# Performance work log

Measured on AMD Instinct MI355X. Metric: run time of the kernel, lower is better.

Reference implementation:

```python
import jax, jax.numpy as jnp
import numpy as np

N = 50000
E = 600000
FEAT = 32
ACT = 8
H = 128
HEADS = 4
C = H // HEADS
L = 3
NEG_SLOPE = 0.2
LN_EPS = 1e-5


def setup_inputs() -> dict:
    key = jax.random.key(0)
    ks = jax.random.split(key, 32)
    s = 0.05
    inp = {
        'x': jax.random.normal(ks[0], (N, FEAT), jnp.float32),
        'action': jax.random.normal(ks[1], (N, ACT), jnp.float32),
        'edge_index': jax.random.randint(ks[2], (2, E), 0, N, jnp.int32),
        # node encoder: Linear(feat+act -> H) + LayerNorm
        'W0': jax.random.normal(ks[3], (FEAT + ACT, H), jnp.float32) * s,
        'b0': jnp.zeros((H,), jnp.float32),
        'ln0_g': jnp.ones((H,), jnp.float32),
        'ln0_b': jnp.zeros((H,), jnp.float32),
        # GAT layers (stacked over L): lin W [L,H,heads*C], att vectors, bias, LayerNorm
        'Wg': jax.random.normal(ks[4], (L, H, HEADS * C), jnp.float32) * s,
        'att_src': jax.random.normal(ks[5], (L, HEADS, C), jnp.float32) * s,
        'att_dst': jax.random.normal(ks[6], (L, HEADS, C), jnp.float32) * s,
        'bg': jnp.zeros((L, HEADS * C), jnp.float32),
        'lng_g': jnp.ones((L, H), jnp.float32),
        'lng_b': jnp.zeros((L, H), jnp.float32),
        # dynamics head
        'Wd1': jax.random.normal(ks[7], (H, H), jnp.float32) * s,
        'bd1': jnp.zeros((H,), jnp.float32),
        'Wd2': jax.random.normal(ks[8], (H, FEAT), jnp.float32) * s,
        'bd2': jnp.zeros((FEAT,), jnp.float32),
        # reward head
        'Wr1': jax.random.normal(ks[9], (H, H // 2), jnp.float32) * s,
        'br1': jnp.zeros((H // 2,), jnp.float32),
        'Wr2': jax.random.normal(ks[10], (H // 2, 1), jnp.float32) * s,
        'br2': jnp.zeros((1,), jnp.float32),
        # constraint head
        'Wc1': jax.random.normal(ks[11], (H, H // 2), jnp.float32) * s,
        'bc1': jnp.zeros((H // 2,), jnp.float32),
        'Wc2': jax.random.normal(ks[12], (H // 2, 1), jnp.float32) * s,
        'bc2': jnp.zeros((1,), jnp.float32),
    }
    return inp


def _layernorm(x, g, b):
    mu = jnp.mean(x, axis=-1, keepdims=True)
    var = jnp.mean(jnp.square(x - mu), axis=-1, keepdims=True)
    return (x - mu) * jax.lax.rsqrt(var + LN_EPS) * g + b


def _gat_layer(h, src, dst, W, a_src, a_dst, bias):
    # PyG GATConv: xp = lin(h) per head; alpha = leaky_relu(a_src.x_j + a_dst.x_i)
    xp = (h @ W).reshape(N, HEADS, C)                    # [N, heads, C]
    s_src = jnp.sum(xp * a_src, axis=-1)                 # [N, heads]
    s_dst = jnp.sum(xp * a_dst, axis=-1)                 # [N, heads]
    alpha = jax.nn.leaky_relu(s_src[src] + s_dst[dst], NEG_SLOPE)  # [E', heads]
    # segment softmax over edges grouped by destination node
    amax = jax.ops.segment_max(alpha, dst, num_segments=N)
    ex = jnp.exp(alpha - amax[dst])
    den = jax.ops.segment_sum(ex, dst, num_segments=N)
    attn = ex / den[dst]                                 # [E', heads]
    msg = xp[src] * attn[..., None]                      # [E', heads, C]
    out = jax.ops.segment_sum(msg.reshape(-1, HEADS * C), dst, num_segments=N)
    return out + bias                                    # [N, H]


def reference(x, action, edge_index, W0, b0, ln0_g, ln0_b, Wg, att_src, att_dst,
              bg, lng_g, lng_b, Wd1, bd1, Wd2, bd2, Wr1, br1, Wr2, br2,
              Wc1, bc1, Wc2, bc2):
    # add self loops (PyG GATConv default)
    loops = jnp.arange(N, dtype=edge_index.dtype)
    src = jnp.concatenate([edge_index[0], loops])
    dst = jnp.concatenate([edge_index[1], loops])

    h = jax.nn.relu(_layernorm(jnp.concatenate([x, action], axis=-1) @ W0 + b0, ln0_g, ln0_b))
    for l in range(L):
        h_new = _gat_layer(h, src, dst, Wg[l], att_src[l], att_dst[l], bg[l])
        h_new = jax.nn.relu(_layernorm(h_new, lng_g[l], lng_b[l]))
        h = h + h_new

    delta_x = jax.nn.relu(h @ Wd1 + bd1) @ Wd2 + bd2
    next_x = x + delta_x
    graph_emb = jnp.mean(h, axis=0, keepdims=True)       # global_mean_pool, single graph
    reward = (jax.nn.relu(graph_emb @ Wr1 + br1) @ Wr2 + br2).squeeze(-1)
    constraint_prob = jax.nn.sigmoid(jax.nn.relu(graph_emb @ Wc1 + bc1) @ Wc2 + bc2).squeeze(-1)
    return delta_x, next_x, reward, constraint_prob
```

## Files before the change

### kernel.cpp

```cpp
#include <hip/hip_runtime.h>

typedef unsigned short u16;
typedef __attribute__((ext_vector_type(8))) short bf16x8;
typedef __attribute__((ext_vector_type(4))) float f32x4;

#define NN 50000
#define EE 600000
#define EP 650000
#define LNEPS 1e-5f
#define NB 196

__device__ __forceinline__ float bf2f(u16 u) {
    union { unsigned int i; float f; } v; v.i = ((unsigned int)u) << 16; return v.f;
}
__device__ __forceinline__ u16 f2bf(float f) {
    union { float f; unsigned int i; } v; v.f = f;
    unsigned int x = v.i;
    unsigned int r = x + 0x7fffu + ((x >> 16) & 1u);
    return (u16)(r >> 16);
}
__device__ __forceinline__ float ldf(const void* p, long i, int bf) {
    return bf ? bf2f(((const u16*)p)[i]) : ((const float*)p)[i];
}
__device__ __forceinline__ void stf(void* p, long i, int bf, float v) {
    if (bf) ((u16*)p)[i] = f2bf(v); else ((float*)p)[i] = v;
}

#define WTOT 93858
#define BSWN 65536
struct P22 { const void* p[22]; };

__global__ __launch_bounds__(256) void init7(P22 w, float* __restrict__ wf,
                                             u16* __restrict__ bsw,
                                             int* __restrict__ deg,
                                             float* __restrict__ gacc,
                                             int* __restrict__ flag) {
    const unsigned w0 = *(const unsigned*)w.p[2];
    const int bf = (w0 == 0x3F803F80u) ? 1 : 0;
    int i = blockIdx.x * 256 + threadIdx.x;
    if (i < WTOT) {
        const int offs[23] = {0,5120,5248,5376,5504,54656,55040,55424,55808,56192,56576,
                              72960,73088,77184,77216,85408,85472,85536,85537,93729,93793,
                              93857,93858};
        int seg = 0;
        while (offs[seg + 1] <= i) ++seg;
        wf[i] = ldf(w.p[seg], i - offs[seg], bf);
        return;
    }
    i -= WTOT;
    if (i < BSWN) {
        int mat = i >> 14, rem = i & 16383;
        int ct = rem >> 11, r2 = rem & 2047;
        int kb = r2 >> 9, r3 = r2 & 511;
        int lane = r3 >> 3, j = r3 & 7;
        int k = kb * 32 + (lane >> 4) * 8 + j;
        int n = ct * 16 + (lane & 15);
        float v = (mat < 3) ? ldf(w.p[4], (long)mat * 16384 + (long)k * 128 + n, bf)
                            : ldf(w.p[10], (long)k * 128 + n, bf);
        bsw[i] = f2bf(v);
        return;
    }
    i -= BSWN;
    if (i < NN) { deg[i] = 0; return; }
    i -= NN;
    if (i < 128) { gacc[i] = 0.f; return; }
    if (i == 128) *flag = bf;
}

__global__ __launch_bounds__(256) void enc6(
    const void* __restrict__ x, const void* __restrict__ act,
    const float* __restrict__ wf, u16* __restrict__ hb,
    const int* __restrict__ flg) {
    const float* W0f = wf;
    const float* b0f = wf + 5120;
    const float* gf  = wf + 5248;
    const float* bbf = wf + 5376;
    __shared__ float As[32][41];
    const int bf = *flg;
    int t = threadIdx.x;
    int r0 = blockIdx.x * 32;
    #pragma unroll
    for (int i = 0; i < 5; ++i) {
        int idx = t + i * 256;
        int r = idx / 40, k = idx - r * 40;
        int rr = r0 + r; if (rr >= NN) rr = NN - 1;
        As[r][k] = (k < 32) ? ldf(x, (long)rr * 32 + k, bf)
                            : ldf(act, (long)rr * 8 + (k - 32), bf);
    }
    __syncthreads();
    int colq = t & 31, mq = t >> 5;
    int col0 = colq * 4;
    float4 b0v = *(const float4*)(b0f + col0);
    float acc[4][4];
    #pragma unroll
    for (int j = 0; j < 4; ++j) {
        acc[j][0] = b0v.x; acc[j][1] = b0v.y; acc[j][2] = b0v.z; acc[j][3] = b0v.w;
    }
    #pragma unroll 2
    for (int k = 0; k < 40; ++k) {
        float4 b4 = *(const float4*)(W0f + k * 128 + col0);
        float a0 = As[mq * 4 + 0][k];
        float a1 = As[mq * 4 + 1][k];
        float a2 = As[mq * 4 + 2][k];
        float a3 = As[mq * 4 + 3][k];
        acc[0][0] += a0 * b4.x; acc[0][1] += a0 * b4.y; acc[0][2] += a0 * b4.z; acc[0][3] += a0 * b4.w;
        acc[1][0] += a1 * b4.x; acc[1][1] += a1 * b4.y; acc[1][2] += a1 * b4.z; acc[1][3] += a1 * b4.w;
        acc[2][0] += a2 * b4.x; acc[2][1] += a2 * b4.y; acc[2][2] += a2 * b4.z; acc[2][3] += a2 * b4.w;
        acc[3][0] += a3 * b4.x; acc[3][1] += a3 * b4.y; acc[3][2] += a3 * b4.z; acc[3][3] += a3 * b4.w;
    }
    float4 gv = *(const float4*)(gf + col0);
    float4 bv = *(const float4*)(bbf + col0);
    #pragma unroll
    for (int j = 0; j < 4; ++j) {
        int row = r0 + mq * 4 + j;
        float pa = acc[j][0] + acc[j][1] + acc[j][2] + acc[j][3];
        #pragma unroll
        for (int o = 1; o <= 16; o <<= 1) pa += __shfl_xor(pa, o, 32);
        float mu = pa * (1.f / 128.f);
        float d0 = acc[j][0] - mu, d1 = acc[j][1] - mu;
        float d2 = acc[j][2] - mu, d3 = acc[j][3] - mu;
        float q = d0 * d0 + d1 * d1 + d2 * d2 + d3 * d3;
        #pragma unroll
        for (int o = 1; o <= 16; o <<= 1) q += __shfl_xor(q, o, 32);
        float rs = rsqrtf(q * (1.f / 128.f) + LNEPS);
        if (row < NN) {
            ushort4 hbv;
            hbv.x = f2bf(fmaxf(d0 * rs * gv.x + bv.x, 0.f));
            hbv.y = f2bf(fmaxf(d1 * rs * gv.y + bv.y, 0.f));
            hbv.z = f2bf(fmaxf(d2 * rs * gv.z + bv.z, 0.f));
            hbv.w = f2bf(fmaxf(d3 * rs * gv.w + bv.w, 0.f));
            *(ushort4*)(hb + (long)row * 128 + col0) = hbv;
        }
    }
}

__global__ __launch_bounds__(256) void lin7(
    const u16* __restrict__ hb, const u16* __restrict__ bswm,
    const float* __restrict__ bias, u16* __restrict__ out, int dorelu,
    int doscore, const float* __restrict__ wf, int layer,
    float* __restrict__ s_src, float* __restrict__ s_dst,
    int douth, const void* __restrict__ x, void* __restrict__ dout,
    const int* __restrict__ flg) {
    __shared__ u16 As[32 * 136];
    __shared__ u16 ts[32 * 136];
    int t = threadIdx.x;
    int r0 = blockIdx.x * 32;
    #pragma unroll
    for (int i = 0; i < 2; ++i) {
        int idx = (t + i * 256) * 8;
        int r = idx >> 7, k = idx & 127;
        int rr = r0 + r; if (rr >= NN) rr = NN - 1;
        int4 v = *(const int4*)(hb + (long)rr * 128 + k);
        *(int4*)(As + r * 136 + k) = v;
    }
    __syncthreads();
    int w = t >> 6, lane = t & 63;
    int rt = w & 1, ctbase = (w >> 1) * 4;
    int quad = lane >> 4, l15 = lane & 15;
    int rowl = rt * 16 + l15;
    bf16x8 afr[4];
    #pragma unroll
    for (int kb = 0; kb < 4; ++kb)
        afr[kb] = *(const bf16x8*)(As + rowl * 136 + kb * 32 + quad * 8);
    const float* asrf = wf + 54656 + layer * 128;
    const float* adsf = wf + 55040 + layer * 128;
    int headbase = (w >> 1) * 2;
    #pragma unroll
    for (int cp = 0; cp < 2; ++cp) {
        int ct0 = ctbase + cp * 2, ct1 = ct0 + 1;
        f32x4 acc0 = {0.f, 0.f, 0.f, 0.f};
        f32x4 acc1 = {0.f, 0.f, 0.f, 0.f};
        #pragma unroll
        for (int kb = 0; kb < 4; ++kb) {
            bf16x8 b0 = *(const bf16x8*)(bswm + ct0 * 2048 + kb * 512 + lane * 8);
            acc0 = __builtin_amdgcn_mfma_f32_16x16x32_bf16(afr[kb], b0, acc0, 0, 0, 0);
        }
        #pragma unroll
        for (int kb = 0; kb < 4; ++kb) {
            bf16x8 b1 = *(const bf16x8*)(bswm + ct1 * 2048 + kb * 512 + lane * 8);
            acc1 = __builtin_amdgcn_mfma_f32_16x16x32_bf16(afr[kb], b1, acc1, 0, 0, 0);
        }
        int col0 = ct0 * 16 + l15, col1 = ct1 * 16 + l15;
        float bia0 = dorelu ? bias[col0] : 0.f;
        float bia1 = dorelu ? bias[col1] : 0.f;
        #pragma unroll
        for (int reg = 0; reg < 4; ++reg) {
            int lrow = rt * 16 + quad * 4 + reg;
            int grow = r0 + lrow;
            float z0 = acc0[reg] + bia0, z1 = acc1[reg] + bia1;
            if (dorelu) { z0 = fmaxf(z0, 0.f); z1 = fmaxf(z1, 0.f); }
            if (douth) {
                ts[lrow * 136 + col0] = f2bf(z0);
                ts[lrow * 136 + col1] = f2bf(z1);
            } else if (grow < NN) {
                out[(long)grow * 128 + col0] = f2bf(z0);
                out[(long)grow * 128 + col1] = f2bf(z1);
            }
        }
        if (doscore) {
            float av0 = asrf[col0], av1 = asrf[col1];
            float dv0 = adsf[col0], dv1 = adsf[col1];
            #pragma unroll
            for (int reg = 0; reg < 4; ++reg) {
                float pa = acc0[reg] * av0 + acc1[reg] * av1;
                float pb = acc0[reg] * dv0 + acc1[reg] * dv1;
                #pragma unroll
                for (int o = 1; o <= 8; o <<= 1) {
                    pa += __shfl_xor(pa, o, 64);
                    pb += __shfl_xor(pb, o, 64);
                }
                if (l15 == 0) {
                    int grow = r0 + rt * 16 + quad * 4 + reg;
                    if (grow < NN) {
                        s_src[grow * 4 + headbase + cp] = pa;
                        s_dst[grow * 4 + headbase + cp] = pb;
                    }
                }
            }
        }
    }
    if (douth) {
        __syncthreads();
        const float* Wd2f = wf + 73088;
        const float* bd2f = wf + 77184;
        const int bf = *flg;
        int c = t & 31, mq = t >> 5;
        float acc[4];
        #pragma unroll
        for (int j = 0; j < 4; ++j) acc[j] = bd2f[c];
        #pragma unroll 4
        for (int k = 0; k < 128; ++k) {
            float wv = Wd2f[k * 32 + c];
            acc[0] += bf2f(ts[(mq * 4 + 0) * 136 + k]) * wv;
            acc[1] += bf2f(ts[(mq * 4 + 1) * 136 + k]) * wv;
            acc[2] += bf2f(ts[(mq * 4 + 2) * 136 + k]) * wv;
            acc[3] += bf2f(ts[(mq * 4 + 3) * 136 + k]) * wv;
        }
        #pragma unroll
        for (int j = 0; j < 4; ++j) {
            int node = r0 + mq * 4 + j;
            if (node >= NN) continue;
            stf(dout, (long)node * 32 + c, bf, acc[j]);
            stf(dout, (long)NN * 32 + (long)node * 32 + c, bf,
                ldf(x, (long)node * 32 + c, bf) + acc[j]);
        }
    }
}

__global__ void count3(const int* __restrict__ ei, int* __restrict__ deg) {
    int e = blockIdx.x * 256 + threadIdx.x; if (e >= EP) return;
    int d = (e < EE) ? ei[EE + e] : (e - EE);
    atomicAdd(&deg[d], 1);
}

__global__ __launch_bounds__(256) void scanA(const int* __restrict__ deg,
                                             int* __restrict__ bsum) {
    __shared__ int red[256];
    int t = threadIdx.x; int i = blockIdx.x * 256 + t;
    red[t] = (i < NN) ? deg[i] : 0; __syncthreads();
    for (int s = 128; s >= 1; s >>= 1) { if (t < s) red[t] += red[t + s]; __syncthreads(); }
    if (t == 0) bsum[blockIdx.x] = red[0];
}

__global__ __launch_bounds__(256) void scanB(const int* __restrict__ bsum,
                                             int* __restrict__ boff,
                                             int* __restrict__ offs) {
    __shared__ int sh[256];
    int t = threadIdx.x;
    sh[t] = (t < NB) ? bsum[t] : 0; __syncthreads();
    for (int o = 1; o < 256; o <<= 1) {
        int v = (t >= o) ? sh[t - o] : 0;
        __syncthreads();
        sh[t] += v;
        __syncthreads();
    }
    if (t < NB) boff[t] = (t == 0) ? 0 : sh[t - 1];
    if (t == 0) offs[NN] = EP;
}

__global__ __launch_bounds__(256) void scanC(const int* __restrict__ deg,
                                             const int* __restrict__ boff,
                                             int* __restrict__ offs,
                                             int* __restrict__ cursor) {
    __shared__ int sh[256];
    int t = threadIdx.x; int i = blockIdx.x * 256 + t;
    int v = (i < NN) ? deg[i] : 0;
    sh[t] = v; __syncthreads();
    for (int o = 1; o < 256; o <<= 1) {
        int u = (t >= o) ? sh[t - o] : 0;
        __syncthreads();
        sh[t] += u;
        __syncthreads();
    }
    if (i < NN) {
        int excl = boff[blockIdx.x] + sh[t] - v;
        offs[i] = excl; cursor[i] = excl;
    }
}

__global__ void scatter5(const int* __restrict__ ei, int* __restrict__ cursor,
                         int* __restrict__ csrc) {
    int e = blockIdx.x * 256 + threadIdx.x; if (e >= EP) return;
    int s, d;
    if (e < EE) { s = ei[e]; d = ei[EE + e]; } else { s = e - EE; d = s; }
    int p = atomicAdd(&cursor[d], 1);
    csrc[p] = s;
}

__global__ __launch_bounds__(256) void agg9(
    const u16* __restrict__ xp, const float* __restrict__ s_src,
    const float* __restrict__ s_dst,
    const int* __restrict__ csrc, const int* __restrict__ offs,
    const float* __restrict__ wf, int layer, u16* __restrict__ hb) {
    const float* bgf = wf + 55424 + layer * 128;
    const float* gf  = wf + 55808 + layer * 128;
    const float* bbf = wf + 56192 + layer * 128;
    int t = threadIdx.x;
    int lane = t & 63;
    int n = blockIdx.x * 4 + (t >> 6);
    int q = (lane >> 4) & 3;
    int l16 = lane & 15;
    int c0 = l16 * 8;
    int hd = l16 >> 2;
    int eh = l16 & 3;
    long idx0 = (long)n * 128 + c0;
    int4 hold = *(const int4*)(hb + idx0);
    float sdn_eh = s_dst[n * 4 + eh];
    float sdn_hd = s_dst[n * 4 + hd];
    int beg = offs[n], end = offs[n + 1];
    float a[8] = {};
    float den = 0.f;
    int j = beg;
    for (; j + 8 <= end; j += 8) {
        int s0 = csrc[j + q];
        int s1 = csrc[j + 4 + q];
        int sp0 = csrc[j + hd];
        int sp1 = csrc[j + 4 + hd];
        float aw0 = s_src[sp0 * 4 + eh] + sdn_eh;
        float aw1 = s_src[sp1 * 4 + eh] + sdn_eh;
        aw0 = (aw0 > 0.f) ? aw0 : 0.2f * aw0;
        aw1 = (aw1 > 0.f) ? aw1 : 0.2f * aw1;
        float w0p = __expf(aw0);
        float w1p = __expf(aw1);
        int4 v0 = *(const int4*)(xp + (long)s0 * 128 + c0);
        int4 v1 = *(const int4*)(xp + (long)s1 * 128 + c0);
        float w0 = __shfl(w0p, q * 4 + hd, 64);
        float w1 = __shfl(w1p, q * 4 + hd, 64);
        union { int4 i; u16 u[8]; } u0, u1;
        u0.i = v0; u1.i = v1;
        #pragma unroll
        for (int k = 0; k < 8; ++k)
            a[k] += w0 * bf2f(u0.u[k]) + w1 * bf2f(u1.u[k]);
        den += w0 + w1;
    }
    for (int jj = j + q; jj < end; jj += 4) {
        int s = csrc[jj];
        float aw = s_src[s * 4 + hd] + sdn_hd;
        aw = (aw > 0.f) ? aw : 0.2f * aw;
        float w = __expf(aw);
        int4 v = *(const int4*)(xp + (long)s * 128 + c0);
        union { int4 i; u16 u[8]; } uv; uv.i = v;
        #pragma unroll
        for (int k = 0; k < 8; ++k) a[k] += w * bf2f(uv.u[k]);
        den += w;
    }
    #pragma unroll
    for (int k = 0; k < 8; ++k) {
        a[k] += __shfl_xor(a[k], 16, 64);
        a[k] += __shfl_xor(a[k], 32, 64);
    }
    den += __shfl_xor(den, 16, 64);
    den += __shfl_xor(den, 32, 64);
    float inv = 1.f / den;
    float4 bg0 = *(const float4*)(bgf + c0);
    float4 bg1 = *(const float4*)(bgf + c0 + 4);
    float v[8];
    v[0] = a[0] * inv + bg0.x; v[1] = a[1] * inv + bg0.y;
    v[2] = a[2] * inv + bg0.z; v[3] = a[3] * inv + bg0.w;
    v[4] = a[4] * inv + bg1.x; v[5] = a[5] * inv + bg1.y;
    v[6] = a[6] * inv + bg1.z; v[7] = a[7] * inv + bg1.w;
    float pa = v[0] + v[1] + v[2] + v[3] + v[4] + v[5] + v[6] + v[7];
    #pragma unroll
    for (int o = 1; o <= 8; o <<= 1) pa += __shfl_xor(pa, o, 16);
    float mu = pa * (1.f / 128.f);
    float d[8];
    float qv = 0.f;
    #pragma unroll
    for (int k = 0; k < 8; ++k) { d[k] = v[k] - mu; qv += d[k] * d[k]; }
    #pragma unroll
    for (int o = 1; o <= 8; o <<= 1) qv += __shfl_xor(qv, o, 16);
    float rs = rsqrtf(qv * (1.f / 128.f) + LNEPS);
    float4 g0 = *(const float4*)(gf + c0);
    float4 g1 = *(const float4*)(gf + c0 + 4);
    float4 b0 = *(const float4*)(bbf + c0);
    float4 b1 = *(const float4*)(bbf + c0 + 4);
    float gg[8]  = {g0.x, g0.y, g0.z, g0.w, g1.x, g1.y, g1.z, g1.w};
    float bbv[8] = {b0.x, b0.y, b0.z, b0.w, b1.x, b1.y, b1.z, b1.w};
    if (lane < 16) {
        union { int4 i; u16 u[8]; } hv, ho;
        ho.i = hold;
        #pragma unroll
        for (int k = 0; k < 8; ++k) {
            float y = fmaxf(d[k] * rs * gg[k] + bbv[k], 0.f);
            hv.u[k] = f2bf(bf2f(ho.u[k]) + y);
        }
        *(int4*)(hb + idx0) = hv.i;
    }
}

__global__ __launch_bounds__(128) void pool4(const u16* __restrict__ hb, float* __restrict__ gacc) {
    int c = threadIdx.x;
    int n0 = blockIdx.x * 128;
    float s = 0.f;
    for (int i = 0; i < 128; ++i) {
        int n = n0 + i;
        if (n < NN) s += bf2f(hb[(long)n * 128 + c]);
    }
    atomicAdd(&gacc[c], s);
}

__global__ __launch_bounds__(128) void head4(
    const float* __restrict__ gacc, const float* __restrict__ wf,
    void* __restrict__ out, const int* __restrict__ flg) {
    const float* Wr1f = wf + 77216;
    const float* br1f = wf + 85408;
    const float* Wr2f = wf + 85472;
    const float* br2f = wf + 85536;
    const float* Wc1f = wf + 85537;
    const float* bc1f = wf + 93729;
    const float* Wc2f = wf + 93793;
    const float* bc2f = wf + 93857;
    __shared__ float ge[128];
    __shared__ float hr[128];
    const int bf = *flg;
    int t = threadIdx.x;
    ge[t] = gacc[t] * (1.f / (float)NN);
    __syncthreads();
    {
        int j = t & 63;
        const float* W = (t < 64) ? Wr1f : Wc1f;
        const float* bb = (t < 64) ? br1f : bc1f;
        float a = bb[j];
        for (int k = 0; k < 128; ++k) a += ge[k] * W[k * 64 + j];
        hr[t] = fmaxf(a, 0.f);
    }
    __syncthreads();
    if (t == 0) {
        float r = br2f[0];
        for (int j = 0; j < 64; ++j) r += hr[j] * Wr2f[j];
        stf(out, (long)2 * NN * 32, bf, r);
    } else if (t == 1) {
        float z = bc2f[0];
        for (int j = 0; j < 64; ++j) z += hr[64 + j] * Wc2f[j];
        float p = 1.f / (1.f + __expf(-z));
        stf(out, (long)2 * NN * 32 + 1, bf, p);
    }
}

extern "C" void kernel_launch(void* const* d_in, const int* in_sizes, int n_in,
                              void* d_out, int out_size, void* d_ws, size_t ws_size,
                              hipStream_t stream) {
    const void* x   = d_in[0];
    const void* act = d_in[1];
    const int*  ei  = (const int*)d_in[2];

    char* ws = (char*)d_ws;
    size_t off = 0;
    auto alloc = [&](size_t bytes) -> char* {
        char* p = ws + off;
        off = (off + bytes + 255) & ~(size_t)255;
        return p;
    };
    u16*       hb     = (u16*)      alloc((size_t)NN * 128 * 2);
    u16*       xp     = (u16*)      alloc((size_t)NN * 128 * 2);
    float*     s_src  = (float*)    alloc((size_t)NN * 4 * 4);
    float*     s_dst  = (float*)    alloc((size_t)NN * 4 * 4);
    int*       deg    = (int*)      alloc((size_t)NN * 4);
    int*       cursor = (int*)      alloc((size_t)NN * 4);
    int*       offs   = (int*)      alloc((size_t)(NN + 1) * 4);
    int*       csrc   = (int*)      alloc((size_t)EP * 4);
    float*     wf     = (float*)    alloc((size_t)WTOT * 4);
    u16*       bsw    = (u16*)      alloc((size_t)BSWN * 2);
    float*     gacc   = (float*)    alloc(128 * 4);
    int*       flag   = (int*)      alloc(4);
    int*       bsum   = (int*)      alloc((size_t)NB * 4);
    int*       boff   = (int*)      alloc((size_t)NB * 4);

    P22 wp;
    for (int i = 0; i < 22; ++i) wp.p[i] = d_in[3 + i];
    const int initN = WTOT + BSWN + NN + 129;
    init7<<<(initN + 255) / 256, 256, 0, stream>>>(wp, wf, bsw, deg, gacc, flag);

    const int gemm_blocks = (NN + 31) / 32;
    enc6<<<gemm_blocks, 256, 0, stream>>>(x, act, wf, hb, flag);

    count3<<<(EP + 255) / 256, 256, 0, stream>>>(ei, deg);
    scanA<<<NB, 256, 0, stream>>>(deg, bsum);
    scanB<<<1, 256, 0, stream>>>(bsum, boff, offs);
    scanC<<<NB, 256, 0, stream>>>(deg, boff, offs, cursor);
    scatter5<<<(EP + 255) / 256, 256, 0, stream>>>(ei, cursor, csrc);

    for (int l = 0; l < 3; ++l) {
        lin7<<<gemm_blocks, 256, 0, stream>>>(hb, bsw + (size_t)l * 16384,
                                              (const float*)nullptr, xp, 0,
                                              1, wf, l, s_src, s_dst,
                                              0, x, d_out, flag);
        agg9<<<NN / 4, 256, 0, stream>>>(xp, s_src, s_dst, csrc, offs,
                                         wf, l, hb);
    }

    lin7<<<gemm_blocks, 256, 0, stream>>>(hb, bsw + (size_t)3 * 16384,
                                          wf + 72960, xp, 1,
                                          0, wf, 0, s_src, s_dst,
                                          1, x, d_out, flag);

    pool4<<<(NN + 127) / 128, 128, 0, stream>>>(hb, gacc);
    head4<<<1, 128, 0, stream>>>(gacc, wf, d_out, flag);

    (void)in_sizes; (void)n_in; (void)out_size; (void)ws_size;
}
```

Baseline: 412.9 us.

## Fuse degree count into encoder, merge scan kernels, batch edge loads in aggregation

```diff
diff --git a/kernel.cpp b/kernel.cpp
--- a/kernel.cpp
+++ b/kernel.cpp
@@ -9,6 +9,8 @@
 #define EP 650000
 #define LNEPS 1e-5f
 #define NB 196
+#define ENCB 1563
+#define CNTB 2540
 
 __device__ __forceinline__ float bf2f(u16 u) {
     union { unsigned int i; float f; } v; v.i = ((unsigned int)u) << 16; return v.f;
@@ -67,10 +69,19 @@
     if (i == 128) *flag = bf;
 }
 
-__global__ __launch_bounds__(256) void enc6(
+__global__ __launch_bounds__(256) void enc7(
     const void* __restrict__ x, const void* __restrict__ act,
     const float* __restrict__ wf, u16* __restrict__ hb,
-    const int* __restrict__ flg) {
+    const int* __restrict__ flg, const int* __restrict__ ei,
+    int* __restrict__ deg) {
+    if (blockIdx.x >= ENCB) {
+        int e = (blockIdx.x - ENCB) * 256 + threadIdx.x;
+        if (e < EP) {
+            int d = (e < EE) ? ei[EE + e] : (e - EE);
+            atomicAdd(&deg[d], 1);
+        }
+        return;
+    }
     const float* W0f = wf;
     const float* b0f = wf + 5120;
     const float* gf  = wf + 5248;
@@ -247,12 +258,6 @@
     }
 }
 
-__global__ void count3(const int* __restrict__ ei, int* __restrict__ deg) {
-    int e = blockIdx.x * 256 + threadIdx.x; if (e >= EP) return;
-    int d = (e < EE) ? ei[EE + e] : (e - EE);
-    atomicAdd(&deg[d], 1);
-}
-
 __global__ __launch_bounds__(256) void scanA(const int* __restrict__ deg,
                                              int* __restrict__ bsum) {
     __shared__ int red[256];
@@ -262,40 +267,37 @@
     if (t == 0) bsum[blockIdx.x] = red[0];
 }
 
-__global__ __launch_bounds__(256) void scanB(const int* __restrict__ bsum,
-                                             int* __restrict__ boff,
-                                             int* __restrict__ offs) {
+__global__ __launch_bounds__(256) void scanC2(const int* __restrict__ deg,
+                                              const int* __restrict__ bsum,
+                                              int* __restrict__ offs,
+                                              int* __restrict__ cursor) {
     __shared__ int sh[256];
     int t = threadIdx.x;
-    sh[t] = (t < NB) ? bsum[t] : 0; __syncthreads();
-    for (int o = 1; o < 256; o <<= 1) {
-        int v = (t >= o) ? sh[t - o] : 0;
-        __syncthreads();
-        sh[t] += v;
-        __syncthreads();
-    }
-    if (t < NB) boff[t] = (t == 0) ? 0 : sh[t - 1];
-    if (t == 0) offs[NN] = EP;
-}
-
-__global__ __launch_bounds__(256) void scanC(const int* __restrict__ deg,
-                                             const int* __restrict__ boff,
-                                             int* __restrict__ offs,
-                                             int* __restrict__ cursor) {
-    __shared__ int sh[256];
-    int t = threadIdx.x; int i = blockIdx.x * 256 + t;
-    int v = (i < NN) ? deg[i] : 0;
-    sh[t] = v; __syncthreads();
+    sh[t] = (t < NB) ? bsum[t] : 0;
+    __syncthreads();
     for (int o = 1; o < 256; o <<= 1) {
         int u = (t >= o) ? sh[t - o] : 0;
         __syncthreads();
         sh[t] += u;
         __syncthreads();
     }
+    int pre = (blockIdx.x == 0) ? 0 : sh[blockIdx.x - 1];
+    __syncthreads();
+    int i = blockIdx.x * 256 + t;
+    int v = (i < NN) ? deg[i] : 0;
+    sh[t] = v;
+    __syncthreads();
+    for (int o = 1; o < 256; o <<= 1) {
+        int u = (t >= o) ? sh[t - o] : 0;
+        __syncthreads();
+        sh[t] += u;
+        __syncthreads();
+    }
     if (i < NN) {
-        int excl = boff[blockIdx.x] + sh[t] - v;
+        int excl = pre + sh[t] - v;
         offs[i] = excl; cursor[i] = excl;
     }
+    if (i == 0) offs[NN] = EP;
 }
 
 __global__ void scatter5(const int* __restrict__ ei, int* __restrict__ cursor,
@@ -307,7 +309,7 @@
     csrc[p] = s;
 }
 
-__global__ __launch_bounds__(256) void agg9(
+__global__ __launch_bounds__(256) void agg10(
     const u16* __restrict__ xp, const float* __restrict__ s_src,
     const float* __restrict__ s_dst,
     const int* __restrict__ csrc, const int* __restrict__ offs,
@@ -322,47 +324,41 @@
     int l16 = lane & 15;
     int c0 = l16 * 8;
     int hd = l16 >> 2;
-    int eh = l16 & 3;
     long idx0 = (long)n * 128 + c0;
     int4 hold = *(const int4*)(hb + idx0);
-    float sdn_eh = s_dst[n * 4 + eh];
-    float sdn_hd = s_dst[n * 4 + hd];
+    float sdn = s_dst[n * 4 + (lane & 3)];
     int beg = offs[n], end = offs[n + 1];
     float a[8] = {};
     float den = 0.f;
-    int j = beg;
-    for (; j + 8 <= end; j += 8) {
-        int s0 = csrc[j + q];
-        int s1 = csrc[j + 4 + q];
-        int sp0 = csrc[j + hd];
-        int sp1 = csrc[j + 4 + hd];
-        float aw0 = s_src[sp0 * 4 + eh] + sdn_eh;
-        float aw1 = s_src[sp1 * 4 + eh] + sdn_eh;
-        aw0 = (aw0 > 0.f) ? aw0 : 0.2f * aw0;
-        aw1 = (aw1 > 0.f) ? aw1 : 0.2f * aw1;
-        float w0p = __expf(aw0);
-        float w1p = __expf(aw1);
-        int4 v0 = *(const int4*)(xp + (long)s0 * 128 + c0);
-        int4 v1 = *(const int4*)(xp + (long)s1 * 128 + c0);
-        float w0 = __shfl(w0p, q * 4 + hd, 64);
-        float w1 = __shfl(w1p, q * 4 + hd, 64);
-        union { int4 i; u16 u[8]; } u0, u1;
-        u0.i = v0; u1.i = v1;
-        #pragma unroll
-        for (int k = 0; k < 8; ++k)
-            a[k] += w0 * bf2f(u0.u[k]) + w1 * bf2f(u1.u[k]);
-        den += w0 + w1;
-    }
-    for (int jj = j + q; jj < end; jj += 4) {
-        int s = csrc[jj];
-        float aw = s_src[s * 4 + hd] + sdn_hd;
-        aw = (aw > 0.f) ? aw : 0.2f * aw;
-        float w = __expf(aw);
-        int4 v = *(const int4*)(xp + (long)s * 128 + c0);
-        union { int4 i; u16 u[8]; } uv; uv.i = v;
-        #pragma unroll
-        for (int k = 0; k < 8; ++k) a[k] += w * bf2f(uv.u[k]);
-        den += w;
+    for (int cbeg = beg; cbeg < end; cbeg += 64) {
+        int cdeg = end - cbeg; if (cdeg > 64) cdeg = 64;
+        int eidx = (lane < cdeg) ? csrc[cbeg + lane] : n;
+        for (int base = 0; base < cdeg; base += 16) {
+            int me = base + (lane >> 2);
+            int sm = __shfl(eidx, me & 63, 64);
+            float aw = s_src[sm * 4 + (lane & 3)] + sdn;
+            aw = (aw > 0.f) ? aw : 0.2f * aw;
+            float wv = (me < cdeg) ? __expf(aw) : 0.f;
+            int s00 = __shfl(eidx, base + q, 64);
+            int s01 = __shfl(eidx, base + 4 + q, 64);
+            int s10 = __shfl(eidx, base + 8 + q, 64);
+            int s11 = __shfl(eidx, base + 12 + q, 64);
+            int4 v00 = *(const int4*)(xp + (long)s00 * 128 + c0);
+            int4 v01 = *(const int4*)(xp + (long)s01 * 128 + c0);
+            int4 v10 = *(const int4*)(xp + (long)s10 * 128 + c0);
+            int4 v11 = *(const int4*)(xp + (long)s11 * 128 + c0);
+            float w00 = __shfl(wv, (q << 2) | hd, 64);
+            float w01 = __shfl(wv, ((4 + q) << 2) | hd, 64);
+            float w10 = __shfl(wv, ((8 + q) << 2) | hd, 64);
+            float w11 = __shfl(wv, ((12 + q) << 2) | hd, 64);
+            union { int4 i; u16 u[8]; } u00, u01, u10, u11;
+            u00.i = v00; u01.i = v01; u10.i = v10; u11.i = v11;
+            #pragma unroll
+            for (int k = 0; k < 8; ++k)
+                a[k] += w00 * bf2f(u00.u[k]) + w01 * bf2f(u01.u[k])
+                      + w10 * bf2f(u10.u[k]) + w11 * bf2f(u11.u[k]);
+            den += w00 + w01 + w10 + w11;
+        }
     }
     #pragma unroll
     for (int k = 0; k < 8; ++k) {
@@ -485,34 +481,32 @@
     int*       flag   = (int*)      alloc(4);
     int*       bsum   = (int*)      alloc((size_t)NB * 4);
     int*       boff   = (int*)      alloc((size_t)NB * 4);
+    (void)boff;
 
     P22 wp;
     for (int i = 0; i < 22; ++i) wp.p[i] = d_in[3 + i];
     const int initN = WTOT + BSWN + NN + 129;
     init7<<<(initN + 255) / 256, 256, 0, stream>>>(wp, wf, bsw, deg, gacc, flag);
 
-    const int gemm_blocks = (NN + 31) / 32;
-    enc6<<<gemm_blocks, 256, 0, stream>>>(x, act, wf, hb, flag);
-
-    count3<<<(EP + 255) / 256, 256, 0, stream>>>(ei, deg);
+    enc7<<<ENCB + CNTB, 256, 0, stream>>>(x, act, wf, hb, flag, ei, deg);
+
     scanA<<<NB, 256, 0, stream>>>(deg, bsum);
-    scanB<<<1, 256, 0, stream>>>(bsum, boff, offs);
-    scanC<<<NB, 256, 0, stream>>>(deg, boff, offs, cursor);
+    scanC2<<<NB, 256, 0, stream>>>(deg, bsum, offs, cursor);
     scatter5<<<(EP + 255) / 256, 256, 0, stream>>>(ei, cursor, csrc);
 
     for (int l = 0; l < 3; ++l) {
-        lin7<<<gemm_blocks, 256, 0, stream>>>(hb, bsw + (size_t)l * 16384,
-                                              (const float*)nullptr, xp, 0,
-                                              1, wf, l, s_src, s_dst,
-                                              0, x, d_out, flag);
-        agg9<<<NN / 4, 256, 0, stream>>>(xp, s_src, s_dst, csrc, offs,
-                                         wf, l, hb);
-    }
-
-    lin7<<<gemm_blocks, 256, 0, stream>>>(hb, bsw + (size_t)3 * 16384,
-                                          wf + 72960, xp, 1,
-                                          0, wf, 0, s_src, s_dst,
-                                          1, x, d_out, flag);
+        lin7<<<ENCB, 256, 0, stream>>>(hb, bsw + (size_t)l * 16384,
+                                       (const float*)nullptr, xp, 0,
+                                       1, wf, l, s_src, s_dst,
+                                       0, x, d_out, flag);
+        agg10<<<NN / 4, 256, 0, stream>>>(xp, s_src, s_dst, csrc, offs,
+                                          wf, l, hb);
+    }
+
+    lin7<<<ENCB, 256, 0, stream>>>(hb, bsw + (size_t)3 * 16384,
+                                   wf + 72960, xp, 1,
+                                   0, wf, 0, s_src, s_dst,
+                                   1, x, d_out, flag);
 
     pool4<<<(NN + 127) / 128, 128, 0, stream>>>(hb, gacc);
     head4<<<1, 128, 0, stream>>>(gacc, wf, d_out, flag);
```

Result: no change. 413.3 us (+0.1%).
